# Optimization experiments

Measured on AMD Instinct MI355X. Metric: run time of the kernel, lower is better.

## Reference

```python
import jax, jax.numpy as jnp
import numpy as np

EPS = 1e-6

def setup_inputs() -> dict:
    key = jax.random.key(0)
    ks = jax.random.split(key, 8)
    B, L, Dm, N, K = 2, 1024, 1024, 64, 4
    Di = Dm * 2  # expand=2
    g = lambda k, shape, scale: jax.random.normal(k, shape, jnp.float32) * scale
    return {
        "x": g(ks[0], (B, L, Dm), 1.0),
        "norm_w": jnp.ones((Dm,), jnp.float32),
        "in_proj_w": g(ks[1], (2 * Di, Dm), 0.02),
        "conv_w": g(ks[2], (Di, 1, K), 0.1),      # depthwise: [out=Di, in/groups=1, K]
        "conv_b": jnp.zeros((Di,), jnp.float32),
        "x_proj_w": g(ks[3], (2 * N, Di), 0.02),
        "dt_w": g(ks[4], (Di, Di), 0.02),
        "dt_b": jnp.ones((Di,), jnp.float32),      # init.constant_(dt_proj.bias, 1.0)
        "A_log": g(ks[5], (Di, N), 1.0) - 4.0,     # normal(mean=-4, std=1)
        "D_param": jnp.ones((Di,), jnp.float32),
        "out_proj_w": g(ks[6], (Dm, Di), 0.02),
    }

def reference(x, norm_w, in_proj_w, conv_w, conv_b, x_proj_w, dt_w, dt_b, A_log, D_param, out_proj_w):
    B, L, Dm = x.shape
    Di = conv_w.shape[0]
    K = conv_w.shape[-1]
    skip = x
    # RMSNorm
    rms = jnp.sqrt(jnp.mean(x * x, axis=-1, keepdims=True) + EPS)
    xn = norm_w * (x / rms)
    # in_proj -> [B,L,2*Di], split into x and res
    xr = xn @ in_proj_w.T
    xi, res = jnp.split(xr, 2, axis=-1)
    # causal depthwise conv1d (pad left K-1, truncate to L == torch pad=K-1 then [:L])
    xc = jax.lax.conv_general_dilated(
        xi.transpose(0, 2, 1), conv_w, window_strides=(1,),
        padding=[(K - 1, 0)], dimension_numbers=("NCH", "OIH", "NCH"),
        feature_group_count=Di)
    xc = (xc + conv_b[None, :, None]).transpose(0, 2, 1)  # [B,L,Di]
    xc = jax.nn.silu(xc)
    # selective scan
    x_dbl = xc @ x_proj_w.T                   # [B,L,2N]; first half (delta) unused, as in source
    _delta, B_ssm = jnp.split(x_dbl, 2, axis=-1)  # B_ssm: [B,L,N]
    dt = jax.nn.softplus(xc @ dt_w.T + dt_b)  # [B,L,Di]
    A = -jnp.exp(A_log.astype(jnp.float32))   # [Di,N]
    N = A.shape[-1]

    def step(h, inp):
        x_t, dt_t, B_t = inp                   # [B,Di],[B,Di],[B,N]
        A_disc = jnp.exp(A[None, :, :] * dt_t[:, :, None])   # [B,Di,N]
        h = A_disc * h + B_t[:, None, :] * x_t[:, :, None]   # [B,Di,N]
        y_t = h.sum(axis=-1) + D_param * x_t                 # [B,Di]
        return h, y_t

    h0 = jnp.zeros((B, Di, N), xc.dtype)
    _, ys = jax.lax.scan(step, h0, (xc.transpose(1, 0, 2), dt.transpose(1, 0, 2), B_ssm.transpose(1, 0, 2)))
    y = ys.transpose(1, 0, 2)                  # [B,L,Di]
    out = (y * jax.nn.silu(res)) @ out_proj_w.T
    return out + skip
```

## Files before the change

kernel.cpp:

```cpp
#include <hip/hip_runtime.h>
#include <hip/hip_bf16.h>
#include <math.h>

#define L_DIM 1024
#define DM 1024
#define DI 2048
#define NS 64

typedef __attribute__((ext_vector_type(8))) short short8;
typedef __attribute__((ext_vector_type(4))) float f32x4;

__device__ __forceinline__ ushort bf16u(float f)
{
    unsigned u = __float_as_uint(f);
    unsigned r = (u + 0x7fffu + ((u >> 16) & 1u)) >> 16;
    return (ushort)r;
}
__device__ __forceinline__ float bf2f(ushort u)
{
    return __uint_as_float((unsigned)u << 16);
}

__device__ __forceinline__ void gld16(const ushort* g, const ushort* l)
{
    __builtin_amdgcn_global_load_lds(
        (const __attribute__((address_space(1))) unsigned int*)g,
        (__attribute__((address_space(3))) unsigned int*)l, 16, 0, 0);
}

__global__ __launch_bounds__(256) void k_rms_xn(const float* __restrict__ x,
    const float* __restrict__ nw, ushort* __restrict__ d)
{
    int row = blockIdx.x;
    const float* xp = x + (size_t)row * DM;
    float4 v = ((const float4*)xp)[threadIdx.x];
    float ss = v.x*v.x + v.y*v.y + v.z*v.z + v.w*v.w;
    #pragma unroll
    for (int m = 32; m; m >>= 1) ss += __shfl_xor(ss, m, 64);
    __shared__ float red[4];
    if ((threadIdx.x & 63) == 0) red[threadIdx.x >> 6] = ss;
    __syncthreads();
    float tot = red[0] + red[1] + red[2] + red[3];
    float ri = rsqrtf(tot * (1.0f / DM) + 1e-6f);
    float4 wv = ((const float4*)nw)[threadIdx.x];
    ((ushort4*)(d + (size_t)row * DM))[threadIdx.x] =
        make_ushort4(bf16u(v.x*ri*wv.x), bf16u(v.y*ri*wv.y),
                     bf16u(v.z*ri*wv.z), bf16u(v.w*ri*wv.w));
}

__device__ __forceinline__ void cast8(const float* __restrict__ s,
                                      ushort* __restrict__ d, int i)
{
    float4 a = ((const float4*)s)[2*i], b = ((const float4*)s)[2*i+1];
    ((ushort4*)d)[2*i]   = make_ushort4(bf16u(a.x), bf16u(a.y), bf16u(a.z), bf16u(a.w));
    ((ushort4*)d)[2*i+1] = make_ushort4(bf16u(b.x), bf16u(b.y), bf16u(b.z), bf16u(b.w));
}
__global__ __launch_bounds__(256) void k_castw(
    const float* __restrict__ s0, ushort* __restrict__ d0,
    const float* __restrict__ s1, ushort* __restrict__ d1,
    const float* __restrict__ s2, ushort* __restrict__ d2,
    const float* __restrict__ s3, ushort* __restrict__ d3)
{
    int i = blockIdx.x * 256 + threadIdx.x;
    if (i < 524288)       cast8(s0, d0, i);
    else if (i < 1048576) cast8(s1, d1, i - 524288);
    else if (i < 1064960) cast8(s2, d2, i - 1048576);
    else                  cast8(s3, d3, i - 1064960);
}

template<int MODE, int BM>
__global__ __launch_bounds__(256) void k_mfma(
    const ushort* __restrict__ Abf, const ushort* __restrict__ Bbf0,
    const ushort* __restrict__ Bbf1, float* __restrict__ C0,
    ushort* __restrict__ C0b, float* __restrict__ C1,
    const float* __restrict__ bias, const float* __restrict__ skip,
    int Kdim, int ldc)
{
    constexpr int NI = (BM == 128) ? 4 : 2;
    constexpr int SA = BM / 32;
    __shared__ __align__(16) ushort As[BM*64];
    __shared__ __align__(16) ushort Bs[128*64];
    const int t = threadIdx.x, w = t >> 6, lane = t & 63;
    const int nwg = gridDim.x * gridDim.y;
    const int orig = blockIdx.y * gridDim.x + blockIdx.x;
    const int swz = (orig & 7) * (nwg >> 3) + (orig >> 3);
    const int nt = swz % gridDim.x, mt = swz / gridDim.x;
    const int mBase = mt * BM, nBase = nt * 128;
    const bool isXP = (MODE == 1) && (nt == 16);
    const ushort* __restrict__ Bbf = isXP ? Bbf1 : Bbf0;
    const int wr = (BM == 128) ? (w >> 1) * 64 : 0;
    const int wc = (BM == 128) ? (w & 1) * 64 : w * 32;
    const int sR = lane >> 3;
    const int sK = ((lane & 7) ^ sR) * 8;

    f32x4 acc[4][NI];
    #pragma unroll
    for (int i = 0; i < 4; ++i)
        #pragma unroll
        for (int j = 0; j < NI; ++j)
            acc[i][j] = (f32x4){0.f, 0.f, 0.f, 0.f};

    for (int kt = 0; kt < Kdim; kt += 64) {
        #pragma unroll
        for (int s = 0; s < SA; ++s) {
            int tr = w*8 + s*32 + sR;
            gld16(Abf + (size_t)(mBase + tr) * Kdim + kt + sK,
                  As + (w*8 + s*32) * 64);
        }
        #pragma unroll
        for (int s = 0; s < 4; ++s) {
            int tr = w*8 + s*32 + sR;
            int gr = isXP ? (tr < 63 ? tr : 63) : (nBase + tr);
            gld16(Bbf + (size_t)gr * Kdim + kt + sK,
                  Bs + (w*8 + s*32) * 64);
        }
        __syncthreads();
        #pragma unroll
        for (int kk = 0; kk < 2; ++kk) {
            short8 af[4], bfr[NI];
            #pragma unroll
            for (int f = 0; f < 4; ++f) {
                int ra = wr + f*16 + (lane & 15);
                int ca = (kk*4 + (lane >> 4)) ^ (ra & 7);
                af[f] = *(const short8*)(As + ra*64 + ca*8);
            }
            #pragma unroll
            for (int f = 0; f < NI; ++f) {
                int rb2 = wc + f*16 + (lane & 15);
                int cb2 = (kk*4 + (lane >> 4)) ^ (rb2 & 7);
                bfr[f] = *(const short8*)(Bs + rb2*64 + cb2*8);
            }
            #pragma unroll
            for (int mi = 0; mi < 4; ++mi)
                #pragma unroll
                for (int ni = 0; ni < NI; ++ni)
                    acc[mi][ni] = __builtin_amdgcn_mfma_f32_16x16x32_bf16(
                        af[mi], bfr[ni], acc[mi][ni], 0, 0, 0);
        }
        __syncthreads();
    }

    const int rb = (lane >> 4) * 4, cbl = lane & 15;
    #pragma unroll
    for (int mi = 0; mi < 4; ++mi) {
        #pragma unroll
        for (int ni = 0; ni < NI; ++ni) {
            int ltcol = wc + ni*16 + cbl;
            int col = nBase + ltcol;
            #pragma unroll
            for (int j = 0; j < 4; ++j) {
                int row = mBase + wr + mi*16 + rb + j;
                float v = acc[mi][ni][j];
                if constexpr (MODE == 0) {
                    C0b[(size_t)row * ldc + col] = bf16u(v);
                } else if constexpr (MODE == 1) {
                    if (isXP) {
                        if (ltcol < NS) C1[(size_t)row * NS + ltcol] = v;
                    } else {
                        float z = v + bias[col];
                        float sp = (z > 20.f) ? z : logf(1.f + expf(z));
                        C0b[(size_t)row * ldc + col] = bf16u(sp);
                    }
                } else {
                    C0[(size_t)row * ldc + col] = v + skip[(size_t)row * ldc + col];
                }
            }
        }
    }
}

__global__ __launch_bounds__(256) void k_conv(const ushort* __restrict__ xrb,
    const float* __restrict__ cw, const float* __restrict__ cb,
    ushort* __restrict__ xcb)
{
    int gid = blockIdx.x * 256 + threadIdx.x;
    int d = (gid & 511) * 4;
    int tt = (gid >> 9) & 1023;
    int b = gid >> 19;
    float4 w[4];
    #pragma unroll
    for (int c = 0; c < 4; ++c) w[c] = *(const float4*)(cw + (size_t)(d + c) * 4);
    float4 acc = *(const float4*)(cb + d);
    const ushort* base = xrb + (size_t)b * L_DIM * (2*DI) + d;
    #pragma unroll
    for (int j = 0; j < 4; ++j) {
        int ti = tt - 3 + j;
        if (ti < 0) continue;
        ushort4 xu = *(const ushort4*)(base + (size_t)ti * (2*DI));
        const float* w0 = (const float*)&w[0];
        const float* w1 = (const float*)&w[1];
        const float* w2 = (const float*)&w[2];
        const float* w3 = (const float*)&w[3];
        acc.x = fmaf(w0[j], bf2f(xu.x), acc.x);
        acc.y = fmaf(w1[j], bf2f(xu.y), acc.y);
        acc.z = fmaf(w2[j], bf2f(xu.z), acc.z);
        acc.w = fmaf(w3[j], bf2f(xu.w), acc.w);
    }
    acc.x = acc.x / (1.f + expf(-acc.x));
    acc.y = acc.y / (1.f + expf(-acc.y));
    acc.z = acc.z / (1.f + expf(-acc.z));
    acc.w = acc.w / (1.f + expf(-acc.w));
    size_t o = (size_t)(b * L_DIM + tt) * DI + d;
    *(ushort4*)(xcb + o) = make_ushort4(bf16u(acc.x), bf16u(acc.y),
                                        bf16u(acc.z), bf16u(acc.w));
}

__global__ __launch_bounds__(256) void k_tr4(const ushort* __restrict__ dtb,
    ushort* __restrict__ dtt, const ushort* __restrict__ xcb,
    ushort* __restrict__ xct)
{
    __shared__ __align__(16) ushort tile[64][72];
    const int r0 = blockIdx.y * 64, c0 = blockIdx.x * 64;
    const int z = blockIdx.z;
    const ushort* s;
    ushort* d;
    if (z < 2) { s = dtb + (size_t)z * L_DIM * DI;       d = dtt + (size_t)z * DI * L_DIM; }
    else       { s = xcb + (size_t)(z-2) * L_DIM * DI;   d = xct + (size_t)(z-2) * DI * L_DIM; }
    const int tx = threadIdx.x & 7, ty = threadIdx.x >> 3;
    #pragma unroll
    for (int p = 0; p < 2; ++p) {
        int r = ty + p*32;
        short8 v = *(const short8*)(s + (size_t)(r0 + r) * DI + c0 + tx*8);
        int g = tx ^ ((r >> 3) & 7);
        *(short8*)&tile[r][g*8] = v;
    }
    __syncthreads();
    #pragma unroll
    for (int p = 0; p < 2; ++p) {
        int crow = ty + p*32;
        ushort o[8];
        #pragma unroll
        for (int j = 0; j < 8; ++j)
            o[j] = tile[tx*8 + j][(((crow >> 3) ^ tx) << 3) + (crow & 7)];
        *(short8*)(d + (size_t)(c0 + crow) * L_DIM + r0 + tx*8) = *(short8*)o;
    }
}

__global__ __launch_bounds__(256) void k_trg(const ushort* __restrict__ yt,
    const ushort* __restrict__ xrb, ushort* __restrict__ ybf)
{
    __shared__ __align__(16) ushort tile[64][72];
    const int r0 = blockIdx.y * 64, c0 = blockIdx.x * 64;
    const int z = blockIdx.z;
    const ushort* s = yt + (size_t)z * DI * L_DIM;
    const int tx = threadIdx.x & 7, ty = threadIdx.x >> 3;
    #pragma unroll
    for (int p = 0; p < 2; ++p) {
        int r = ty + p*32;
        short8 v = *(const short8*)(s + (size_t)(r0 + r) * L_DIM + c0 + tx*8);
        int g = tx ^ ((r >> 3) & 7);
        *(short8*)&tile[r][g*8] = v;
    }
    __syncthreads();
    #pragma unroll
    for (int p = 0; p < 2; ++p) {
        int crow = ty + p*32;
        int row = z * L_DIM + c0 + crow;
        ushort4 gu0 = *(const ushort4*)(xrb + (size_t)row * (2*DI) + DI + r0 + tx*8);
        ushort4 gu1 = *(const ushort4*)(xrb + (size_t)row * (2*DI) + DI + r0 + tx*8 + 4);
        ushort o[8];
        const ushort* gp = (const ushort*)&gu0;
        #pragma unroll
        for (int j = 0; j < 8; ++j) {
            float yv = bf2f(tile[tx*8 + j][(((crow >> 3) ^ tx) << 3) + (crow & 7)]);
            float g = bf2f(j < 4 ? ((const ushort*)&gu0)[j] : ((const ushort*)&gu1)[j-4]);
            o[j] = bf16u(yv * g / (1.f + expf(-g)));
        }
        (void)gp;
        *(short8*)(ybf + (size_t)row * DI + r0 + tx*8) = *(short8*)o;
    }
}

__device__ __forceinline__ float rl(float v, int lane)
{
    return __int_as_float(__builtin_amdgcn_readlane(__float_as_int(v), lane));
}
__device__ __forceinline__ float exp2_fast(float x)
{
    float r;
    asm("v_exp_f32 %0, %1" : "=v"(r) : "v"(x));
    return r;
}

__global__ __launch_bounds__(256) void k_scan9(const ushort* __restrict__ dtt,
    const ushort* __restrict__ xct, const float* __restrict__ Bss,
    const float* __restrict__ A_log, const float* __restrict__ Dp,
    ushort* __restrict__ yt)
{
    __shared__ float Bsh[64][68];
    __shared__ __align__(16) float Psh[4][64][8];
    const int lane = threadIdx.x & 63;
    const int widx = threadIdx.x >> 6;
    const int b = blockIdx.x >> 9;
    const int d = (blockIdx.x & 511) * 4 + widx;
    const float aL2 = -expf(A_log[(size_t)d * NS + lane]) * 1.44269504f;
    const float Dv = Dp[d];
    const ushort* dtp = dtt + ((size_t)b * DI + d) * L_DIM;
    const ushort* xcp = xct + ((size_t)b * DI + d) * L_DIM;
    const float* Bp  = Bss + (size_t)b * L_DIM * NS;
    ushort* yp = yt + ((size_t)b * DI + d) * L_DIM;
    const int lr = threadIdx.x >> 2;
    const int lc = (threadIdx.x & 3) * 16;
    const int pg = lane >> 3;
    const bool pwrite = (lane & 7) == 7;
    float h = 0.f;

    for (int t0 = 0; t0 < L_DIM; t0 += 64) {
        const float* bsrc = Bp + (size_t)(t0 + lr) * NS + lc;
        float4 b0 = *(const float4*)(bsrc);
        float4 b1 = *(const float4*)(bsrc + 4);
        float4 b2 = *(const float4*)(bsrc + 8);
        float4 b3 = *(const float4*)(bsrc + 12);
        float dt_v = bf2f(dtp[t0 + lane]);
        float xc_v = bf2f(xcp[t0 + lane]);
        __syncthreads();
        *(float4*)&Bsh[lr][lc]      = b0;
        *(float4*)&Bsh[lr][lc + 4]  = b1;
        *(float4*)&Bsh[lr][lc + 8]  = b2;
        *(float4*)&Bsh[lr][lc + 12] = b3;
        __syncthreads();
        #pragma unroll
        for (int q = 0; q < 64; q += 4) {
            float Bv0 = Bsh[q+0][lane];
            float Bv1 = Bsh[q+1][lane];
            float Bv2 = Bsh[q+2][lane];
            float Bv3 = Bsh[q+3][lane];
            float s0, s1, s2, s3;
            {
                float p, ad;
                p  = rl(xc_v, q+0) * Bv0;
                ad = exp2_fast(aL2 * rl(dt_v, q+0));
                h = fmaf(ad, h, p); s0 = h;
                p  = rl(xc_v, q+1) * Bv1;
                ad = exp2_fast(aL2 * rl(dt_v, q+1));
                h = fmaf(ad, h, p); s1 = h;
                p  = rl(xc_v, q+2) * Bv2;
                ad = exp2_fast(aL2 * rl(dt_v, q+2));
                h = fmaf(ad, h, p); s2 = h;
                p  = rl(xc_v, q+3) * Bv3;
                ad = exp2_fast(aL2 * rl(dt_v, q+3));
                h = fmaf(ad, h, p); s3 = h;
            }
            asm("v_add_f32_dpp %0, %0, %0 row_shr:1 row_mask:0xf bank_mask:0xf\n\t"
                "v_add_f32_dpp %1, %1, %1 row_shr:1 row_mask:0xf bank_mask:0xf\n\t"
                "v_add_f32_dpp %2, %2, %2 row_shr:1 row_mask:0xf bank_mask:0xf\n\t"
                "v_add_f32_dpp %3, %3, %3 row_shr:1 row_mask:0xf bank_mask:0xf\n\t"
                "v_add_f32_dpp %0, %0, %0 row_shr:2 row_mask:0xf bank_mask:0xf\n\t"
                "v_add_f32_dpp %1, %1, %1 row_shr:2 row_mask:0xf bank_mask:0xf\n\t"
                "v_add_f32_dpp %2, %2, %2 row_shr:2 row_mask:0xf bank_mask:0xf\n\t"
                "v_add_f32_dpp %3, %3, %3 row_shr:2 row_mask:0xf bank_mask:0xf\n\t"
                "v_add_f32_dpp %0, %0, %0 row_shr:4 row_mask:0xf bank_mask:0xf\n\t"
                "v_add_f32_dpp %1, %1, %1 row_shr:4 row_mask:0xf bank_mask:0xf\n\t"
                "v_add_f32_dpp %2, %2, %2 row_shr:4 row_mask:0xf bank_mask:0xf\n\t"
                "v_add_f32_dpp %3, %3, %3 row_shr:4 row_mask:0xf bank_mask:0xf"
                : "+v"(s0), "+v"(s1), "+v"(s2), "+v"(s3));
            if (pwrite) {
                Psh[widx][q+0][pg] = s0;
                Psh[widx][q+1][pg] = s1;
                Psh[widx][q+2][pg] = s2;
                Psh[widx][q+3][pg] = s3;
            }
        }
        asm volatile("s_waitcnt lgkmcnt(0)" ::: "memory");
        __builtin_amdgcn_sched_barrier(0);
        float4 p0 = *(const float4*)&Psh[widx][lane][0];
        float4 p1 = *(const float4*)&Psh[widx][lane][4];
        float sum = ((p0.x + p0.y) + (p0.z + p0.w))
                  + ((p1.x + p1.y) + (p1.z + p1.w));
        yp[t0 + lane] = bf16u(fmaf(Dv, xc_v, sum));
    }
}

extern "C" void kernel_launch(void* const* d_in, const int* in_sizes, int n_in,
                              void* d_out, int out_size, void* d_ws, size_t ws_size,
                              hipStream_t stream)
{
    const float* x        = (const float*)d_in[0];
    const float* norm_w   = (const float*)d_in[1];
    const float* in_projw = (const float*)d_in[2];
    const float* conv_w   = (const float*)d_in[3];
    const float* conv_b   = (const float*)d_in[4];
    const float* x_projw  = (const float*)d_in[5];
    const float* dt_w     = (const float*)d_in[6];
    const float* dt_b     = (const float*)d_in[7];
    const float* A_log    = (const float*)d_in[8];
    const float* D_param  = (const float*)d_in[9];
    const float* out_projw= (const float*)d_in[10];
    float* out = (float*)d_out;

    ushort* wsu = (ushort*)d_ws;
    ushort* xr_bf  = wsu;
    ushort* xc_bf  = xr_bf + (size_t)8*1024*1024;
    ushort* dtb_bf = xc_bf + (size_t)4*1024*1024;
    ushort* dtt_bf = dtb_bf + (size_t)4*1024*1024;
    ushort* xct_bf = dtt_bf + (size_t)4*1024*1024;
    ushort* xn_bf  = xct_bf + (size_t)4*1024*1024;
    ushort* xpw_bf = xn_bf + (size_t)2*1024*1024;
    ushort* opw_bf = xpw_bf + 131072;
    float*  Bss    = (float*)(opw_bf + (size_t)2*1024*1024);
    ushort* inpw_bf = dtt_bf;
    ushort* dtw_bf  = xct_bf;
    ushort* y_bf    = xc_bf;
    ushort* yt_bf   = dtb_bf;

    k_castw<<<5184, 256, 0, stream>>>(in_projw, inpw_bf, dt_w, dtw_bf,
                                      x_projw + (size_t)64*2048, xpw_bf,
                                      out_projw, opw_bf);
    k_rms_xn<<<2048, 256, 0, stream>>>(x, norm_w, xn_bf);
    k_mfma<0,128><<<dim3(32, 16), 256, 0, stream>>>(xn_bf, inpw_bf, nullptr,
                                                nullptr, xr_bf, nullptr,
                                                nullptr, nullptr, 1024, 4096);
    k_conv<<<4096, 256, 0, stream>>>(xr_bf, conv_w, conv_b, xc_bf);
    k_mfma<1,128><<<dim3(17, 16), 256, 0, stream>>>(xc_bf, dtw_bf, xpw_bf,
                                                nullptr, dtb_bf, Bss,
                                                dt_b, nullptr, 2048, 2048);
    k_tr4<<<dim3(32, 16, 4), 256, 0, stream>>>(dtb_bf, dtt_bf, xc_bf, xct_bf);
    k_scan9<<<1024, 256, 0, stream>>>(dtt_bf, xct_bf, Bss, A_log, D_param, yt_bf);
    k_trg<<<dim3(16, 32, 2), 256, 0, stream>>>(yt_bf, xr_bf, y_bf);
    k_mfma<2,64><<<dim3(8, 32), 256, 0, stream>>>(y_bf, opw_bf, nullptr,
                                               out, nullptr, nullptr,
                                               nullptr, x, 2048, 1024);
}
```

Before: 253.9 us.

## Write dt transposed from GEMM epilogue and broadcast scan inputs via LDS

The dt-projection GEMM epilogue now stores softplus(dt) directly in the transposed [B,Di,L] layout with 4-element vector stores. This removes the dt half of the separate transpose kernel, which now only transposes xc. Separately, the scan kernel stages each wave's dt and xc values in shared memory and reads them as float4, replacing per-step readlane broadcasts. The trade-off is a strided epilogue store pattern and extra LDS traffic in the scan.

```diff
diff --git a/kernel.cpp b/kernel.cpp
--- a/kernel.cpp
+++ b/kernel.cpp
@@ -147,23 +147,35 @@
         for (int ni = 0; ni < NI; ++ni) {
             int ltcol = wc + ni*16 + cbl;
             int col = nBase + ltcol;
-            #pragma unroll
-            for (int j = 0; j < 4; ++j) {
-                int row = mBase + wr + mi*16 + rb + j;
-                float v = acc[mi][ni][j];
-                if constexpr (MODE == 0) {
-                    C0b[(size_t)row * ldc + col] = bf16u(v);
-                } else if constexpr (MODE == 1) {
-                    if (isXP) {
-                        if (ltcol < NS) C1[(size_t)row * NS + ltcol] = v;
-                    } else {
-                        float z = v + bias[col];
-                        float sp = (z > 20.f) ? z : logf(1.f + expf(z));
-                        C0b[(size_t)row * ldc + col] = bf16u(sp);
+            int row0 = mBase + wr + mi*16 + rb;
+            if constexpr (MODE == 0) {
+                #pragma unroll
+                for (int j = 0; j < 4; ++j)
+                    C0b[(size_t)(row0+j) * ldc + col] = bf16u(acc[mi][ni][j]);
+            } else if constexpr (MODE == 1) {
+                if (isXP) {
+                    if (ltcol < NS) {
+                        #pragma unroll
+                        for (int j = 0; j < 4; ++j)
+                            C1[(size_t)(row0+j) * NS + ltcol] = acc[mi][ni][j];
                     }
                 } else {
-                    C0[(size_t)row * ldc + col] = v + skip[(size_t)row * ldc + col];
+                    ushort o[4];
+                    #pragma unroll
+                    for (int j = 0; j < 4; ++j) {
+                        float z = acc[mi][ni][j] + bias[col];
+                        float sp = (z > 20.f) ? z : logf(1.f + expf(z));
+                        o[j] = bf16u(sp);
+                    }
+                    int b_ = row0 >> 10, trow = row0 & 1023;
+                    *(ushort4*)(C0b + ((size_t)b_ * DI + col) * L_DIM + trow) =
+                        *(ushort4*)o;
                 }
+            } else {
+                #pragma unroll
+                for (int j = 0; j < 4; ++j)
+                    C0[(size_t)(row0+j) * ldc + col] =
+                        acc[mi][ni][j] + skip[(size_t)(row0+j) * ldc + col];
             }
         }
     }
@@ -205,17 +217,14 @@
                                         bf16u(acc.z), bf16u(acc.w));
 }
 
-__global__ __launch_bounds__(256) void k_tr4(const ushort* __restrict__ dtb,
-    ushort* __restrict__ dtt, const ushort* __restrict__ xcb,
+__global__ __launch_bounds__(256) void k_tr2(const ushort* __restrict__ xcb,
     ushort* __restrict__ xct)
 {
     __shared__ __align__(16) ushort tile[64][72];
     const int r0 = blockIdx.y * 64, c0 = blockIdx.x * 64;
     const int z = blockIdx.z;
-    const ushort* s;
-    ushort* d;
-    if (z < 2) { s = dtb + (size_t)z * L_DIM * DI;       d = dtt + (size_t)z * DI * L_DIM; }
-    else       { s = xcb + (size_t)(z-2) * L_DIM * DI;   d = xct + (size_t)(z-2) * DI * L_DIM; }
+    const ushort* s = xcb + (size_t)z * L_DIM * DI;
+    ushort* d = xct + (size_t)z * DI * L_DIM;
     const int tx = threadIdx.x & 7, ty = threadIdx.x >> 3;
     #pragma unroll
     for (int p = 0; p < 2; ++p) {
@@ -259,22 +268,16 @@
         ushort4 gu0 = *(const ushort4*)(xrb + (size_t)row * (2*DI) + DI + r0 + tx*8);
         ushort4 gu1 = *(const ushort4*)(xrb + (size_t)row * (2*DI) + DI + r0 + tx*8 + 4);
         ushort o[8];
-        const ushort* gp = (const ushort*)&gu0;
         #pragma unroll
         for (int j = 0; j < 8; ++j) {
             float yv = bf2f(tile[tx*8 + j][(((crow >> 3) ^ tx) << 3) + (crow & 7)]);
             float g = bf2f(j < 4 ? ((const ushort*)&gu0)[j] : ((const ushort*)&gu1)[j-4]);
             o[j] = bf16u(yv * g / (1.f + expf(-g)));
         }
-        (void)gp;
         *(short8*)(ybf + (size_t)row * DI + r0 + tx*8) = *(short8*)o;
     }
 }
 
-__device__ __forceinline__ float rl(float v, int lane)
-{
-    return __int_as_float(__builtin_amdgcn_readlane(__float_as_int(v), lane));
-}
 __device__ __forceinline__ float exp2_fast(float x)
 {
     float r;
@@ -282,13 +285,15 @@
     return r;
 }
 
-__global__ __launch_bounds__(256) void k_scan9(const ushort* __restrict__ dtt,
+__global__ __launch_bounds__(256) void k_scan10(const ushort* __restrict__ dtt,
     const ushort* __restrict__ xct, const float* __restrict__ Bss,
     const float* __restrict__ A_log, const float* __restrict__ Dp,
     ushort* __restrict__ yt)
 {
     __shared__ float Bsh[64][68];
     __shared__ __align__(16) float Psh[4][64][8];
+    __shared__ __align__(16) float Dsh[4][64];
+    __shared__ __align__(16) float Xsh[4][64];
     const int lane = threadIdx.x & 63;
     const int widx = threadIdx.x >> 6;
     const int b = blockIdx.x >> 9;
@@ -318,9 +323,13 @@
         *(float4*)&Bsh[lr][lc + 4]  = b1;
         *(float4*)&Bsh[lr][lc + 8]  = b2;
         *(float4*)&Bsh[lr][lc + 12] = b3;
+        Dsh[widx][lane] = dt_v;
+        Xsh[widx][lane] = xc_v;
         __syncthreads();
         #pragma unroll
         for (int q = 0; q < 64; q += 4) {
+            float4 dt4 = *(const float4*)&Dsh[widx][q];
+            float4 xc4 = *(const float4*)&Xsh[widx][q];
             float Bv0 = Bsh[q+0][lane];
             float Bv1 = Bsh[q+1][lane];
             float Bv2 = Bsh[q+2][lane];
@@ -328,17 +337,17 @@
             float s0, s1, s2, s3;
             {
                 float p, ad;
-                p  = rl(xc_v, q+0) * Bv0;
-                ad = exp2_fast(aL2 * rl(dt_v, q+0));
+                p  = xc4.x * Bv0;
+                ad = exp2_fast(aL2 * dt4.x);
                 h = fmaf(ad, h, p); s0 = h;
-                p  = rl(xc_v, q+1) * Bv1;
-                ad = exp2_fast(aL2 * rl(dt_v, q+1));
+                p  = xc4.y * Bv1;
+                ad = exp2_fast(aL2 * dt4.y);
                 h = fmaf(ad, h, p); s1 = h;
-                p  = rl(xc_v, q+2) * Bv2;
-                ad = exp2_fast(aL2 * rl(dt_v, q+2));
+                p  = xc4.z * Bv2;
+                ad = exp2_fast(aL2 * dt4.z);
                 h = fmaf(ad, h, p); s2 = h;
-                p  = rl(xc_v, q+3) * Bv3;
-                ad = exp2_fast(aL2 * rl(dt_v, q+3));
+                p  = xc4.w * Bv3;
+                ad = exp2_fast(aL2 * dt4.w);
                 h = fmaf(ad, h, p); s3 = h;
             }
             asm("v_add_f32_dpp %0, %0, %0 row_shr:1 row_mask:0xf bank_mask:0xf\n\t"
@@ -412,10 +421,10 @@
                                                 nullptr, nullptr, 1024, 4096);
     k_conv<<<4096, 256, 0, stream>>>(xr_bf, conv_w, conv_b, xc_bf);
     k_mfma<1,128><<<dim3(17, 16), 256, 0, stream>>>(xc_bf, dtw_bf, xpw_bf,
-                                                nullptr, dtb_bf, Bss,
+                                                nullptr, dtt_bf, Bss,
                                                 dt_b, nullptr, 2048, 2048);
-    k_tr4<<<dim3(32, 16, 4), 256, 0, stream>>>(dtb_bf, dtt_bf, xc_bf, xct_bf);
-    k_scan9<<<1024, 256, 0, stream>>>(dtt_bf, xct_bf, Bss, A_log, D_param, yt_bf);
+    k_tr2<<<dim3(32, 16, 2), 256, 0, stream>>>(xc_bf, xct_bf);
+    k_scan10<<<1024, 256, 0, stream>>>(dtt_bf, xct_bf, Bss, A_log, D_param, yt_bf);
     k_trg<<<dim3(16, 32, 2), 256, 0, stream>>>(yt_bf, xr_bf, y_bf);
     k_mfma<2,64><<<dim3(8, 32), 256, 0, stream>>>(y_bf, opw_bf, nullptr,
                                                out, nullptr, nullptr,
```

After: 234.2 us. 7.7% less time.
